# Performance work log

Hardware: AMD Instinct MI355X
Metric: run time of the kernel (lower is better)

Reference implementation:

```python
import jax, jax.numpy as jnp
import numpy as np

N_EMBD = 768
HEAD_SIZE = 72
SEQ_LEN = 512
BATCH = 64

def setup_inputs() -> dict:
    key = jax.random.key(0)
    kx, kk, kq, kv = jax.random.split(key, 4)
    # Linear weights stored as [in, out] for x @ W; torch Linear init ~ U(-1/sqrt(in), 1/sqrt(in))
    bound = 1.0 / np.sqrt(N_EMBD)
    x = jax.random.normal(kx, (BATCH, SEQ_LEN, N_EMBD), dtype=jnp.float32)
    Wk = jax.random.uniform(kk, (N_EMBD, HEAD_SIZE), minval=-bound, maxval=bound, dtype=jnp.float32)
    Wq = jax.random.uniform(kq, (N_EMBD, HEAD_SIZE), minval=-bound, maxval=bound, dtype=jnp.float32)
    Wv = jax.random.uniform(kv, (N_EMBD, HEAD_SIZE), minval=-bound, maxval=bound, dtype=jnp.float32)
    return {"x": x, "Wk": Wk, "Wq": Wq, "Wv": Wv}

def reference(x, Wk, Wq, Wv):
    # Single causal self-attention head (dropout in eval mode = identity).
    k = x @ Wk  # [B, T, H]
    q = x @ Wq  # [B, T, H]
    v = x @ Wv  # [B, T, H]
    scale = k.shape[-1] ** (-0.5)
    scores = jnp.einsum('bth,bsh->bts', q, k) * scale  # [B, T, T]
    T = scores.shape[-1]
    causal = jnp.tril(jnp.ones((T, T), dtype=bool))
    scores = jnp.where(causal, scores, -jnp.inf)
    attn = jax.nn.softmax(scores, axis=-1)
    out = jnp.einsum('bts,bsh->bth', attn, v)  # [B, T, H]
    return out
```

## Files before the change

kernel.cpp:

```cpp
#include <hip/hip_runtime.h>


typedef short bf16x8 __attribute__((ext_vector_type(8)));
typedef float f32x4 __attribute__((ext_vector_type(4)));

#define DEVI __device__ __forceinline__

DEVI unsigned f2bf(float f) {
  unsigned u = __builtin_bit_cast(unsigned, f);
  return (u + 0x7fffu + ((u >> 16) & 1u)) >> 16;
}
DEVI unsigned pk2(float a, float b) { return f2bf(a) | (f2bf(b) << 16); }

DEVI void async16(void* lds, const void* g) {
  __builtin_amdgcn_global_load_lds(
      (const __attribute__((address_space(1))) unsigned int*)g,
      (__attribute__((address_space(3))) unsigned int*)lds, 16, 0, 0);
}

__global__ __launch_bounds__(256) void cast_w_k(const float* __restrict__ Wk,
                                                const float* __restrict__ Wq,
                                                const float* __restrict__ Wv,
                                                unsigned short* __restrict__ wbt) {
  __shared__ float ldsT[72][65];
  const int mat = blockIdx.x / 12, kc = blockIdx.x % 12;
  const float* W = (mat == 0) ? Wk : (mat == 1) ? Wq : Wv;
  const float sc = (mat == 1) ? 0.11785113019775793f : 1.0f;
  const float* src = W + kc * 64 * 72;
  for (int i = threadIdx.x; i < 1152; i += 256) {
    float4 d = *(const float4*)(src + i * 4);
    int e = i * 4;
    ldsT[e % 72][e / 72] = d.x;
    ldsT[(e + 1) % 72][(e + 1) / 72] = d.y;
    ldsT[(e + 2) % 72][(e + 2) / 72] = d.z;
    ldsT[(e + 3) % 72][(e + 3) / 72] = d.w;
  }
  __syncthreads();
  for (int c = threadIdx.x; c < 640; c += 256) {
    int h = c >> 3, kb = (c & 7) * 8;
    uint4 o = {0u, 0u, 0u, 0u};
    if (h < 72) {
      const float* rowp = &ldsT[h][kb];
      o.x = pk2(rowp[0] * sc, rowp[1] * sc);
      o.y = pk2(rowp[2] * sc, rowp[3] * sc);
      o.z = pk2(rowp[4] * sc, rowp[5] * sc);
      o.w = pk2(rowp[6] * sc, rowp[7] * sc);
    }
    *(uint4*)(wbt + ((size_t)mat * 80 + h) * 768 + kc * 64 + kb) = o;
  }
}

struct ProjSmem {
  union {
    struct { short x[128 * 64]; short w[240 * 64]; } s;
    short t[80 * 136];
  };
};

__global__ __launch_bounds__(256, 2) void proj_k(
    const float* __restrict__ x, const unsigned short* __restrict__ wbt,
    unsigned short* __restrict__ Kg, unsigned short* __restrict__ Qg,
    unsigned short* __restrict__ Vt) {
  __shared__ __align__(16) ProjSmem sm;
  const int row0 = blockIdx.x * 128;
  const int tid = threadIdx.x, wave = tid >> 6, lane = tid & 63;
  const int quad = lane >> 4, l16 = lane & 15;
  const int lrow = lane >> 3, lcb = lane & 7;

  f32x4 acc[2][15] = {};

  for (int k0 = 0; k0 < 768; k0 += 64) {
#pragma unroll
    for (int i = 0; i < 8; ++i) {
      int inst = i * 4 + wave;
      if (inst < 30) {
        int r = inst * 8 + lrow;
        async16(&sm.s.w[inst * 512], wbt + (size_t)r * 768 + k0 + (lcb ^ lrow) * 8);
      }
    }
#pragma unroll
    for (int i = 0; i < 4; ++i) {
      int task = tid + 256 * i;
      int row = task >> 3, cb = task & 7;
      const float* g = x + (size_t)(row0 + row) * 768 + k0 + cb * 8;
      float4 a = *(const float4*)g;
      float4 c = *(const float4*)(g + 4);
      uint4 o = {pk2(a.x, a.y), pk2(a.z, a.w), pk2(c.x, c.y), pk2(c.z, c.w)};
      *(uint4*)&sm.s.x[row * 64 + ((cb ^ (row & 7)) * 8)] = o;
    }
    __syncthreads();
#pragma unroll
    for (int ks = 0; ks < 2; ++ks) {
      const int pblk = ((ks << 2) | quad) ^ (l16 & 7);
      bf16x8 af[2];
#pragma unroll
      for (int mt = 0; mt < 2; ++mt)
        af[mt] = *(const bf16x8*)&sm.s.x[(wave * 32 + mt * 16 + l16) * 64 + pblk * 8];
#pragma unroll
      for (int nt = 0; nt < 15; ++nt) {
        bf16x8 bf = *(const bf16x8*)&sm.s.w[(nt * 16 + l16) * 64 + pblk * 8];
        acc[0][nt] = __builtin_amdgcn_mfma_f32_16x16x32_bf16(af[0], bf, acc[0][nt], 0, 0, 0);
        acc[1][nt] = __builtin_amdgcn_mfma_f32_16x16x32_bf16(af[1], bf, acc[1][nt], 0, 0, 0);
      }
    }
    __syncthreads();
  }

#pragma unroll
  for (int gsel = 0; gsel < 2; ++gsel) {
    unsigned short* G = gsel ? Qg : Kg;
#pragma unroll
    for (int mt = 0; mt < 2; ++mt)
#pragma unroll
      for (int r = 0; r < 4; ++r) {
        size_t row = (size_t)row0 + wave * 32 + mt * 16 + quad * 4 + r;
        unsigned short* p = G + row * 104;
#pragma unroll
        for (int nt = 0; nt < 5; ++nt)
          p[nt * 16 + l16] = (unsigned short)f2bf(acc[mt][gsel * 5 + nt][r]);
        p[80 + l16] = 0;
        if (l16 < 8) p[96 + l16] = 0;
      }
  }
#pragma unroll
  for (int mt = 0; mt < 2; ++mt)
#pragma unroll
    for (int nt = 0; nt < 5; ++nt)
#pragma unroll
      for (int r = 0; r < 4; ++r)
        sm.t[(nt * 16 + l16) * 136 + wave * 32 + mt * 16 + quad * 4 + r] =
            (short)f2bf(acc[mt][10 + nt][r]);
  __syncthreads();
  int b = blockIdx.x >> 2, t0 = (blockIdx.x & 3) * 128;
  const uint4 ones = {0x3F803F80u, 0x3F803F80u, 0x3F803F80u, 0x3F803F80u};
  for (int c = tid; c < 1280; c += 256) {
    int hr = c >> 4, tc = (c & 15) * 8;
    uint4 d = *(const uint4*)&sm.t[hr * 136 + tc];
    if (hr == 72) d = ones;
    *(uint4*)(Vt + ((size_t)b * 80 + hr) * 512 + t0 + tc) = d;
  }
}

__global__ __launch_bounds__(256, 4) void attn_k(
    const unsigned short* __restrict__ Qg, const unsigned short* __restrict__ Kg,
    const unsigned short* __restrict__ Vt, float* __restrict__ out) {
  __shared__ __align__(16) short lk[64 * 104];
  __shared__ __align__(16) short lv[80 * 64];
  __shared__ __align__(16) short lp[4][16 * 72];

  int idx = (blockIdx.x < 256) ? blockIdx.x : 767 - blockIdx.x;
  const int qb = 7 - (idx >> 6), b = idx & 63;
  const int tid = threadIdx.x, wave = tid >> 6, lane = tid & 63;
  const int quad = lane >> 4, l16 = lane & 15;
  const int lrow = lane >> 3, lcb = lane & 7;
  const int trow0 = qb * 64 + wave * 16;

  bf16x8 qf[3];
#pragma unroll
  for (int kt = 0; kt < 3; ++kt)
    qf[kt] = *(const bf16x8*)(Qg + ((size_t)b * 512 + trow0 + l16) * 104 + kt * 32 + quad * 8);

  f32x4 o[5] = {};

  for (int kb = 0; kb <= qb; ++kb) {
    const int s0 = kb * 64;
    const bool diag = (kb == qb);
    const int nact = diag ? (wave + 1) : 4;

#pragma unroll
    for (int j = 0; j < 4; ++j) {
      int inst = j * 4 + wave;
      if (inst < 13)
        async16(&lk[inst * 512], Kg + ((size_t)b * 512 + s0) * 104 + inst * 512 + lane * 8);
    }
    for (int j = wave; j < 10; j += 4) {
      int r = j * 8 + lrow;
      async16(&lv[j * 512], Vt + ((size_t)b * 80 + r) * 512 + s0 + (lcb ^ lrow) * 8);
    }
    __syncthreads();

    f32x4 sacc[4] = {};
#pragma unroll
    for (int kt = 0; kt < 3; ++kt)
      for (int nt = 0; nt < nact; ++nt) {
        bf16x8 kf = *(const bf16x8*)&lk[(nt * 16 + l16) * 104 + kt * 32 + quad * 8];
        sacc[nt] = __builtin_amdgcn_mfma_f32_16x16x32_bf16(qf[kt], kf, sacc[nt], 0, 0, 0);
      }
    if (diag) {
      int nt = wave;
#pragma unroll
      for (int r = 0; r < 4; ++r) {
        int t = trow0 + quad * 4 + r;
        if (s0 + nt * 16 + l16 > t) sacc[nt][r] = -1e30f;
      }
    }
#pragma unroll
    for (int nt = 0; nt < 4; ++nt)
#pragma unroll
      for (int r = 0; r < 4; ++r) {
        float p = (nt < nact) ? __expf(sacc[nt][r]) : 0.0f;
        lp[wave][(quad * 4 + r) * 72 + nt * 16 + l16] = (short)f2bf(p);
      }
#pragma unroll
    for (int ks = 0; ks < 2; ++ks) {
      bf16x8 pf = *(const bf16x8*)&lp[wave][l16 * 72 + ks * 32 + quad * 8];
      const int pblk = ((ks << 2) | quad) ^ (l16 & 7);
#pragma unroll
      for (int nt = 0; nt < 5; ++nt) {
        bf16x8 vf = *(const bf16x8*)&lv[(nt * 16 + l16) * 64 + pblk * 8];
        o[nt] = __builtin_amdgcn_mfma_f32_16x16x32_bf16(pf, vf, o[nt], 0, 0, 0);
      }
    }
    __syncthreads();
  }

#pragma unroll
  for (int r = 0; r < 4; ++r) {
    float l = __shfl(o[4][r], (lane & 48) | 8, 64);
    float inv = 1.0f / l;
    size_t t = (size_t)b * 512 + trow0 + quad * 4 + r;
#pragma unroll
    for (int nt = 0; nt < 5; ++nt) {
      int h = nt * 16 + l16;
      if (h < 72) out[t * 72 + h] = o[nt][r] * inv;
    }
  }
}

extern "C" void kernel_launch(void* const* d_in, const int* in_sizes, int n_in,
                              void* d_out, int out_size, void* d_ws, size_t ws_size,
                              hipStream_t stream) {
  const float* x  = (const float*)d_in[0];
  const float* Wk = (const float*)d_in[1];
  const float* Wq = (const float*)d_in[2];
  const float* Wv = (const float*)d_in[3];
  float* out = (float*)d_out;

  char* ws = (char*)d_ws;
  unsigned short* Kg  = (unsigned short*)(ws);
  unsigned short* Qg  = (unsigned short*)(ws + 6815744);
  unsigned short* Vt  = (unsigned short*)(ws + 13631488);
  unsigned short* wbt = (unsigned short*)(ws + 18874368);

  cast_w_k<<<36, 256, 0, stream>>>(Wk, Wq, Wv, wbt);
  proj_k<<<256, 256, 0, stream>>>(x, wbt, Kg, Qg, Vt);
  attn_k<<<512, 256, 0, stream>>>(Qg, Kg, Vt, out);
}
```

Baseline: 193.5 us.

## Halve projection row tile and double attention key block to 128

The projection kernel now handles 64 rows per block instead of 128, launching 512 blocks so more of the GPU is busy. The attention kernel walks keys in 128-wide blocks, which halves the loop iterations and barriers, and uses a 16-way XOR swizzle for V in LDS. On the diagonal it skips MFMAs and loads past the causal limit. The cost is more LDS per attention block with occupancy lowered to 2 blocks per SM, and the projection reuses each weight tile over fewer rows.

```diff
diff --git a/kernel.cpp b/kernel.cpp
--- a/kernel.cpp
+++ b/kernel.cpp
@@ -52,8 +52,8 @@
 
 struct ProjSmem {
   union {
-    struct { short x[128 * 64]; short w[240 * 64]; } s;
-    short t[80 * 136];
+    struct { short x[64 * 64]; short w[240 * 64]; } s;
+    short t[80 * 72];
   };
 };
 
@@ -62,12 +62,12 @@
     unsigned short* __restrict__ Kg, unsigned short* __restrict__ Qg,
     unsigned short* __restrict__ Vt) {
   __shared__ __align__(16) ProjSmem sm;
-  const int row0 = blockIdx.x * 128;
+  const int row0 = blockIdx.x * 64;
   const int tid = threadIdx.x, wave = tid >> 6, lane = tid & 63;
   const int quad = lane >> 4, l16 = lane & 15;
   const int lrow = lane >> 3, lcb = lane & 7;
 
-  f32x4 acc[2][15] = {};
+  f32x4 acc[15] = {};
 
   for (int k0 = 0; k0 < 768; k0 += 64) {
 #pragma unroll
@@ -79,7 +79,7 @@
       }
     }
 #pragma unroll
-    for (int i = 0; i < 4; ++i) {
+    for (int i = 0; i < 2; ++i) {
       int task = tid + 256 * i;
       int row = task >> 3, cb = task & 7;
       const float* g = x + (size_t)(row0 + row) * 768 + k0 + cb * 8;
@@ -92,15 +92,11 @@
 #pragma unroll
     for (int ks = 0; ks < 2; ++ks) {
       const int pblk = ((ks << 2) | quad) ^ (l16 & 7);
-      bf16x8 af[2];
-#pragma unroll
-      for (int mt = 0; mt < 2; ++mt)
-        af[mt] = *(const bf16x8*)&sm.s.x[(wave * 32 + mt * 16 + l16) * 64 + pblk * 8];
+      bf16x8 af = *(const bf16x8*)&sm.s.x[(wave * 16 + l16) * 64 + pblk * 8];
 #pragma unroll
       for (int nt = 0; nt < 15; ++nt) {
         bf16x8 bf = *(const bf16x8*)&sm.s.w[(nt * 16 + l16) * 64 + pblk * 8];
-        acc[0][nt] = __builtin_amdgcn_mfma_f32_16x16x32_bf16(af[0], bf, acc[0][nt], 0, 0, 0);
-        acc[1][nt] = __builtin_amdgcn_mfma_f32_16x16x32_bf16(af[1], bf, acc[1][nt], 0, 0, 0);
+        acc[nt] = __builtin_amdgcn_mfma_f32_16x16x32_bf16(af, bf, acc[nt], 0, 0, 0);
       }
     }
     __syncthreads();
@@ -110,49 +106,44 @@
   for (int gsel = 0; gsel < 2; ++gsel) {
     unsigned short* G = gsel ? Qg : Kg;
 #pragma unroll
-    for (int mt = 0; mt < 2; ++mt)
-#pragma unroll
-      for (int r = 0; r < 4; ++r) {
-        size_t row = (size_t)row0 + wave * 32 + mt * 16 + quad * 4 + r;
-        unsigned short* p = G + row * 104;
-#pragma unroll
-        for (int nt = 0; nt < 5; ++nt)
-          p[nt * 16 + l16] = (unsigned short)f2bf(acc[mt][gsel * 5 + nt][r]);
-        p[80 + l16] = 0;
-        if (l16 < 8) p[96 + l16] = 0;
-      }
-  }
-#pragma unroll
-  for (int mt = 0; mt < 2; ++mt)
-#pragma unroll
-    for (int nt = 0; nt < 5; ++nt)
-#pragma unroll
-      for (int r = 0; r < 4; ++r)
-        sm.t[(nt * 16 + l16) * 136 + wave * 32 + mt * 16 + quad * 4 + r] =
-            (short)f2bf(acc[mt][10 + nt][r]);
+    for (int r = 0; r < 4; ++r) {
+      size_t row = (size_t)row0 + wave * 16 + quad * 4 + r;
+      unsigned short* p = G + row * 104;
+#pragma unroll
+      for (int nt = 0; nt < 5; ++nt)
+        p[nt * 16 + l16] = (unsigned short)f2bf(acc[gsel * 5 + nt][r]);
+      p[80 + l16] = 0;
+      if (l16 < 8) p[96 + l16] = 0;
+    }
+  }
+#pragma unroll
+  for (int nt = 0; nt < 5; ++nt)
+#pragma unroll
+    for (int r = 0; r < 4; ++r)
+      sm.t[(nt * 16 + l16) * 72 + wave * 16 + quad * 4 + r] =
+          (short)f2bf(acc[10 + nt][r]);
   __syncthreads();
-  int b = blockIdx.x >> 2, t0 = (blockIdx.x & 3) * 128;
+  int b = blockIdx.x >> 3, t0 = (blockIdx.x & 7) * 64;
   const uint4 ones = {0x3F803F80u, 0x3F803F80u, 0x3F803F80u, 0x3F803F80u};
-  for (int c = tid; c < 1280; c += 256) {
-    int hr = c >> 4, tc = (c & 15) * 8;
-    uint4 d = *(const uint4*)&sm.t[hr * 136 + tc];
+  for (int c = tid; c < 640; c += 256) {
+    int hr = c >> 3, tc = (c & 7) * 8;
+    uint4 d = *(const uint4*)&sm.t[hr * 72 + tc];
     if (hr == 72) d = ones;
     *(uint4*)(Vt + ((size_t)b * 80 + hr) * 512 + t0 + tc) = d;
   }
 }
 
-__global__ __launch_bounds__(256, 4) void attn_k(
+__global__ __launch_bounds__(256, 2) void attn_k(
     const unsigned short* __restrict__ Qg, const unsigned short* __restrict__ Kg,
     const unsigned short* __restrict__ Vt, float* __restrict__ out) {
-  __shared__ __align__(16) short lk[64 * 104];
-  __shared__ __align__(16) short lv[80 * 64];
-  __shared__ __align__(16) short lp[4][16 * 72];
+  __shared__ __align__(16) short lk[128 * 104];
+  __shared__ __align__(16) short lv[80 * 128];
+  __shared__ __align__(16) short lp[4][16 * 136];
 
   int idx = (blockIdx.x < 256) ? blockIdx.x : 767 - blockIdx.x;
   const int qb = 7 - (idx >> 6), b = idx & 63;
   const int tid = threadIdx.x, wave = tid >> 6, lane = tid & 63;
   const int quad = lane >> 4, l16 = lane & 15;
-  const int lrow = lane >> 3, lcb = lane & 7;
   const int trow0 = qb * 64 + wave * 16;
 
   bf16x8 qf[3];
@@ -162,55 +153,66 @@
 
   f32x4 o[5] = {};
 
-  for (int kb = 0; kb <= qb; ++kb) {
-    const int s0 = kb * 64;
-    const bool diag = (kb == qb);
-    const int nact = diag ? (wave + 1) : 4;
-
-#pragma unroll
-    for (int j = 0; j < 4; ++j) {
+  const int nkb = (qb >> 1) + 1;
+  for (int kb = 0; kb < nkb; ++kb) {
+    const int s0 = kb * 128;
+    const bool diag = (kb == (qb >> 1));
+    const int nact = diag ? ((qb & 1) * 4 + wave + 1) : 8;
+    const int kslim = diag ? ((nact + 1) >> 1) : 4;
+    const int nKinst = (diag && !(qb & 1)) ? 13 : 26;
+
+#pragma unroll
+    for (int j = 0; j < 7; ++j) {
       int inst = j * 4 + wave;
-      if (inst < 13)
+      if (inst < nKinst)
         async16(&lk[inst * 512], Kg + ((size_t)b * 512 + s0) * 104 + inst * 512 + lane * 8);
     }
-    for (int j = wave; j < 10; j += 4) {
-      int r = j * 8 + lrow;
-      async16(&lv[j * 512], Vt + ((size_t)b * 80 + r) * 512 + s0 + (lcb ^ lrow) * 8);
-    }
-    __syncthreads();
-
-    f32x4 sacc[4] = {};
+#pragma unroll
+    for (int j = 0; j < 5; ++j) {
+      int inst = j * 4 + wave;
+      int r = inst * 4 + (lane >> 4);
+      int cb = lane & 15;
+      async16(&lv[inst * 512],
+              Vt + ((size_t)b * 80 + r) * 512 + s0 + ((cb ^ (r & 15)) * 8));
+    }
+    __syncthreads();
+
+    f32x4 sacc[8] = {};
 #pragma unroll
     for (int kt = 0; kt < 3; ++kt)
-      for (int nt = 0; nt < nact; ++nt) {
-        bf16x8 kf = *(const bf16x8*)&lk[(nt * 16 + l16) * 104 + kt * 32 + quad * 8];
-        sacc[nt] = __builtin_amdgcn_mfma_f32_16x16x32_bf16(qf[kt], kf, sacc[nt], 0, 0, 0);
-      }
+#pragma unroll
+      for (int nt = 0; nt < 8; ++nt)
+        if (nt < nact) {
+          bf16x8 kf = *(const bf16x8*)&lk[(nt * 16 + l16) * 104 + kt * 32 + quad * 8];
+          sacc[nt] = __builtin_amdgcn_mfma_f32_16x16x32_bf16(qf[kt], kf, sacc[nt], 0, 0, 0);
+        }
     if (diag) {
-      int nt = wave;
-#pragma unroll
-      for (int r = 0; r < 4; ++r) {
-        int t = trow0 + quad * 4 + r;
-        if (s0 + nt * 16 + l16 > t) sacc[nt][r] = -1e30f;
-      }
-    }
-#pragma unroll
-    for (int nt = 0; nt < 4; ++nt)
+#pragma unroll
+      for (int nt = 0; nt < 8; ++nt)
+        if (nt == nact - 1)
+#pragma unroll
+          for (int r = 0; r < 4; ++r) {
+            int t = trow0 + quad * 4 + r;
+            if (s0 + nt * 16 + l16 > t) sacc[nt][r] = -1e30f;
+          }
+    }
+#pragma unroll
+    for (int nt = 0; nt < 8; ++nt)
 #pragma unroll
       for (int r = 0; r < 4; ++r) {
         float p = (nt < nact) ? __expf(sacc[nt][r]) : 0.0f;
-        lp[wave][(quad * 4 + r) * 72 + nt * 16 + l16] = (short)f2bf(p);
-      }
-#pragma unroll
-    for (int ks = 0; ks < 2; ++ks) {
-      bf16x8 pf = *(const bf16x8*)&lp[wave][l16 * 72 + ks * 32 + quad * 8];
-      const int pblk = ((ks << 2) | quad) ^ (l16 & 7);
-#pragma unroll
-      for (int nt = 0; nt < 5; ++nt) {
-        bf16x8 vf = *(const bf16x8*)&lv[(nt * 16 + l16) * 64 + pblk * 8];
-        o[nt] = __builtin_amdgcn_mfma_f32_16x16x32_bf16(pf, vf, o[nt], 0, 0, 0);
-      }
-    }
+        lp[wave][(quad * 4 + r) * 136 + nt * 16 + l16] = (short)f2bf(p);
+      }
+#pragma unroll
+    for (int ks = 0; ks < 4; ++ks)
+      if (ks < kslim) {
+        bf16x8 pf = *(const bf16x8*)&lp[wave][l16 * 136 + ks * 32 + quad * 8];
+#pragma unroll
+        for (int nt = 0; nt < 5; ++nt) {
+          bf16x8 vf = *(const bf16x8*)&lv[(nt * 16 + l16) * 128 + (((ks << 2) | quad) ^ l16) * 8];
+          o[nt] = __builtin_amdgcn_mfma_f32_16x16x32_bf16(pf, vf, o[nt], 0, 0, 0);
+        }
+      }
     __syncthreads();
   }
 
@@ -243,6 +245,6 @@
   unsigned short* wbt = (unsigned short*)(ws + 18874368);
 
   cast_w_k<<<36, 256, 0, stream>>>(Wk, Wq, Wv, wbt);
-  proj_k<<<256, 256, 0, stream>>>(x, wbt, Kg, Qg, Vt);
+  proj_k<<<512, 256, 0, stream>>>(x, wbt, Kg, Qg, Vt);
   attn_k<<<512, 256, 0, stream>>>(Qg, Kg, Vt, out);
 }
```

Measured after the change: 201.4 us. +4.1%, slower.

## Load x fragments directly from global in projection, stage weights in larger K chunks

Applied to the files above, without the earlier changes.

The projection kernel no longer stages x through LDS. Each wave now loads its x rows straight from global memory into MFMA fragments, converting them to bf16 in registers. Weights are staged in 256-wide K chunks with a 32-way XOR swizzle, so there are 3 outer iterations instead of 12 and far fewer barriers. The cost is a much larger LDS footprint (about 120KB), which drops occupancy to one block per CU. The x loads also become short, non-coalesced, latency-exposed global reads issued right before the MFMAs.

```diff
diff --git a/kernel.cpp b/kernel.cpp
--- a/kernel.cpp
+++ b/kernel.cpp
@@ -11,6 +11,11 @@
   return (u + 0x7fffu + ((u >> 16) & 1u)) >> 16;
 }
 DEVI unsigned pk2(float a, float b) { return f2bf(a) | (f2bf(b) << 16); }
+
+DEVI bf16x8 pack8(float4 a, float4 c) {
+  uint4 o = {pk2(a.x, a.y), pk2(a.z, a.w), pk2(c.x, c.y), pk2(c.z, c.w)};
+  return __builtin_bit_cast(bf16x8, o);
+}
 
 DEVI void async16(void* lds, const void* g) {
   __builtin_amdgcn_global_load_lds(
@@ -52,12 +57,12 @@
 
 struct ProjSmem {
   union {
-    struct { short x[128 * 64]; short w[240 * 64]; } s;
+    short w[240 * 256];
     short t[80 * 136];
   };
 };
 
-__global__ __launch_bounds__(256, 2) void proj_k(
+__global__ __launch_bounds__(256, 1) void proj_k(
     const float* __restrict__ x, const unsigned short* __restrict__ wbt,
     unsigned short* __restrict__ Kg, unsigned short* __restrict__ Qg,
     unsigned short* __restrict__ Vt) {
@@ -65,40 +70,35 @@
   const int row0 = blockIdx.x * 128;
   const int tid = threadIdx.x, wave = tid >> 6, lane = tid & 63;
   const int quad = lane >> 4, l16 = lane & 15;
-  const int lrow = lane >> 3, lcb = lane & 7;
+  const int wr = wave * 32;
 
   f32x4 acc[2][15] = {};
 
-  for (int k0 = 0; k0 < 768; k0 += 64) {
-#pragma unroll
-    for (int i = 0; i < 8; ++i) {
-      int inst = i * 4 + wave;
-      if (inst < 30) {
-        int r = inst * 8 + lrow;
-        async16(&sm.s.w[inst * 512], wbt + (size_t)r * 768 + k0 + (lcb ^ lrow) * 8);
-      }
-    }
-#pragma unroll
-    for (int i = 0; i < 4; ++i) {
-      int task = tid + 256 * i;
-      int row = task >> 3, cb = task & 7;
-      const float* g = x + (size_t)(row0 + row) * 768 + k0 + cb * 8;
-      float4 a = *(const float4*)g;
-      float4 c = *(const float4*)(g + 4);
-      uint4 o = {pk2(a.x, a.y), pk2(a.z, a.w), pk2(c.x, c.y), pk2(c.z, c.w)};
-      *(uint4*)&sm.s.x[row * 64 + ((cb ^ (row & 7)) * 8)] = o;
-    }
-    __syncthreads();
-#pragma unroll
-    for (int ks = 0; ks < 2; ++ks) {
-      const int pblk = ((ks << 2) | quad) ^ (l16 & 7);
+  for (int kc = 0; kc < 3; ++kc) {
+    const int kbase = kc * 256;
+#pragma unroll
+    for (int j = 0; j < 30; ++j) {
+      int inst = j * 4 + wave;
+      int r = 2 * inst + (lane >> 5);
+      int cb = lane & 31;
+      async16(&sm.w[inst * 512],
+              wbt + (size_t)r * 768 + kbase + ((cb ^ (r & 31)) * 8));
+    }
+    __syncthreads();
+#pragma unroll
+    for (int ks = 0; ks < 8; ++ks) {
       bf16x8 af[2];
 #pragma unroll
-      for (int mt = 0; mt < 2; ++mt)
-        af[mt] = *(const bf16x8*)&sm.s.x[(wave * 32 + mt * 16 + l16) * 64 + pblk * 8];
+      for (int mt = 0; mt < 2; ++mt) {
+        const float* g = x + (size_t)(row0 + wr + mt * 16 + l16) * 768 +
+                         kbase + ks * 32 + quad * 8;
+        af[mt] = pack8(*(const float4*)g, *(const float4*)(g + 4));
+      }
 #pragma unroll
       for (int nt = 0; nt < 15; ++nt) {
-        bf16x8 bf = *(const bf16x8*)&sm.s.w[(nt * 16 + l16) * 64 + pblk * 8];
+        int row = nt * 16 + l16;
+        bf16x8 bf = *(const bf16x8*)&sm.w[row * 256 +
+                                          (((ks * 4 + quad) ^ (row & 31)) * 8)];
         acc[0][nt] = __builtin_amdgcn_mfma_f32_16x16x32_bf16(af[0], bf, acc[0][nt], 0, 0, 0);
         acc[1][nt] = __builtin_amdgcn_mfma_f32_16x16x32_bf16(af[1], bf, acc[1][nt], 0, 0, 0);
       }
@@ -113,7 +113,7 @@
     for (int mt = 0; mt < 2; ++mt)
 #pragma unroll
       for (int r = 0; r < 4; ++r) {
-        size_t row = (size_t)row0 + wave * 32 + mt * 16 + quad * 4 + r;
+        size_t row = (size_t)row0 + wr + mt * 16 + quad * 4 + r;
         unsigned short* p = G + row * 104;
 #pragma unroll
         for (int nt = 0; nt < 5; ++nt)
@@ -128,7 +128,7 @@
     for (int nt = 0; nt < 5; ++nt)
 #pragma unroll
       for (int r = 0; r < 4; ++r)
-        sm.t[(nt * 16 + l16) * 136 + wave * 32 + mt * 16 + quad * 4 + r] =
+        sm.t[(nt * 16 + l16) * 136 + wr + mt * 16 + quad * 4 + r] =
             (short)f2bf(acc[mt][10 + nt][r]);
   __syncthreads();
   int b = blockIdx.x >> 2, t0 = (blockIdx.x & 3) * 128;
```

After: 205.8 us. 6.4% more time.

## Halve projection row tile and split waves across M and N

Applied to the files above, without the earlier changes.

The projection kernel now processes 64 rows per block instead of 128 and splits the four waves into two row groups and two column groups of output tiles. The grid doubles to 512 blocks, giving more parallelism and lower per-wave register use on a GPU with many CUs. In exchange, the weight tile is loaded into LDS by twice as many blocks, adding global and L2 traffic. The epilogue is reworked so each wave writes its own K, Q or V columns, with V transposed through a smaller LDS buffer.

```diff
diff --git a/kernel.cpp b/kernel.cpp
--- a/kernel.cpp
+++ b/kernel.cpp
@@ -52,8 +52,8 @@
 
 struct ProjSmem {
   union {
-    struct { short x[128 * 64]; short w[240 * 64]; } s;
-    short t[80 * 136];
+    struct { short x[64 * 64]; short w[240 * 64]; } s;
+    short t[80 * 72];
   };
 };
 
@@ -62,12 +62,14 @@
     unsigned short* __restrict__ Kg, unsigned short* __restrict__ Qg,
     unsigned short* __restrict__ Vt) {
   __shared__ __align__(16) ProjSmem sm;
-  const int row0 = blockIdx.x * 128;
+  const int row0 = blockIdx.x * 64;
   const int tid = threadIdx.x, wave = tid >> 6, lane = tid & 63;
   const int quad = lane >> 4, l16 = lane & 15;
   const int lrow = lane >> 3, lcb = lane & 7;
-
-  f32x4 acc[2][15] = {};
+  const int mg = wave >> 1, ng = wave & 1;
+  const int ntile0 = ng * 8, ntn = ng ? 7 : 8;
+
+  f32x4 acc[2][8] = {};
 
   for (int k0 = 0; k0 < 768; k0 += 64) {
 #pragma unroll
@@ -79,7 +81,7 @@
       }
     }
 #pragma unroll
-    for (int i = 0; i < 4; ++i) {
+    for (int i = 0; i < 2; ++i) {
       int task = tid + 256 * i;
       int row = task >> 3, cb = task & 7;
       const float* g = x + (size_t)(row0 + row) * 768 + k0 + cb * 8;
@@ -95,47 +97,48 @@
       bf16x8 af[2];
 #pragma unroll
       for (int mt = 0; mt < 2; ++mt)
-        af[mt] = *(const bf16x8*)&sm.s.x[(wave * 32 + mt * 16 + l16) * 64 + pblk * 8];
-#pragma unroll
-      for (int nt = 0; nt < 15; ++nt) {
-        bf16x8 bf = *(const bf16x8*)&sm.s.w[(nt * 16 + l16) * 64 + pblk * 8];
-        acc[0][nt] = __builtin_amdgcn_mfma_f32_16x16x32_bf16(af[0], bf, acc[0][nt], 0, 0, 0);
-        acc[1][nt] = __builtin_amdgcn_mfma_f32_16x16x32_bf16(af[1], bf, acc[1][nt], 0, 0, 0);
-      }
-    }
-    __syncthreads();
-  }
-
-#pragma unroll
-  for (int gsel = 0; gsel < 2; ++gsel) {
-    unsigned short* G = gsel ? Qg : Kg;
-#pragma unroll
-    for (int mt = 0; mt < 2; ++mt)
-#pragma unroll
-      for (int r = 0; r < 4; ++r) {
-        size_t row = (size_t)row0 + wave * 32 + mt * 16 + quad * 4 + r;
-        unsigned short* p = G + row * 104;
-#pragma unroll
-        for (int nt = 0; nt < 5; ++nt)
-          p[nt * 16 + l16] = (unsigned short)f2bf(acc[mt][gsel * 5 + nt][r]);
-        p[80 + l16] = 0;
-        if (l16 < 8) p[96 + l16] = 0;
-      }
-  }
+        af[mt] = *(const bf16x8*)&sm.s.x[(mg * 32 + mt * 16 + l16) * 64 + pblk * 8];
+#pragma unroll
+      for (int j = 0; j < 8; ++j)
+        if (j < ntn) {
+          int nt = ntile0 + j;
+          bf16x8 bf = *(const bf16x8*)&sm.s.w[(nt * 16 + l16) * 64 + pblk * 8];
+          acc[0][j] = __builtin_amdgcn_mfma_f32_16x16x32_bf16(af[0], bf, acc[0][j], 0, 0, 0);
+          acc[1][j] = __builtin_amdgcn_mfma_f32_16x16x32_bf16(af[1], bf, acc[1][j], 0, 0, 0);
+        }
+    }
+    __syncthreads();
+  }
+
 #pragma unroll
   for (int mt = 0; mt < 2; ++mt)
 #pragma unroll
-    for (int nt = 0; nt < 5; ++nt)
-#pragma unroll
-      for (int r = 0; r < 4; ++r)
-        sm.t[(nt * 16 + l16) * 136 + wave * 32 + mt * 16 + quad * 4 + r] =
-            (short)f2bf(acc[mt][10 + nt][r]);
+    for (int r = 0; r < 4; ++r) {
+      int lrow64 = mg * 32 + mt * 16 + quad * 4 + r;
+      size_t grow = (size_t)row0 + lrow64;
+#pragma unroll
+      for (int j = 0; j < 8; ++j)
+        if (j < ntn) {
+          int nt = ntile0 + j;
+          float v = acc[mt][j][r];
+          if (nt < 5) {
+            Kg[grow * 104 + nt * 16 + l16] = (unsigned short)f2bf(v);
+          } else if (nt < 10) {
+            Qg[grow * 104 + (nt - 5) * 16 + l16] = (unsigned short)f2bf(v);
+          } else {
+            sm.t[((nt - 10) * 16 + l16) * 72 + lrow64] = (short)f2bf(v);
+          }
+        }
+      unsigned short* p = (ng ? Qg : Kg) + grow * 104;
+      p[80 + l16] = 0;
+      if (l16 < 8) p[96 + l16] = 0;
+    }
   __syncthreads();
-  int b = blockIdx.x >> 2, t0 = (blockIdx.x & 3) * 128;
+  int b = blockIdx.x >> 3, t0 = (blockIdx.x & 7) * 64;
   const uint4 ones = {0x3F803F80u, 0x3F803F80u, 0x3F803F80u, 0x3F803F80u};
-  for (int c = tid; c < 1280; c += 256) {
-    int hr = c >> 4, tc = (c & 15) * 8;
-    uint4 d = *(const uint4*)&sm.t[hr * 136 + tc];
+  for (int c = tid; c < 640; c += 256) {
+    int hr = c >> 3, tc = (c & 7) * 8;
+    uint4 d = *(const uint4*)&sm.t[hr * 72 + tc];
     if (hr == 72) d = ones;
     *(uint4*)(Vt + ((size_t)b * 80 + hr) * 512 + t0 + tc) = d;
   }
@@ -243,6 +246,6 @@
   unsigned short* wbt = (unsigned short*)(ws + 18874368);
 
   cast_w_k<<<36, 256, 0, stream>>>(Wk, Wq, Wv, wbt);
-  proj_k<<<256, 256, 0, stream>>>(x, wbt, Kg, Qg, Vt);
+  proj_k<<<512, 256, 0, stream>>>(x, wbt, Kg, Qg, Vt);
   attn_k<<<512, 256, 0, stream>>>(Qg, Kg, Vt, out);
 }
```

Measured after the change: 193.0 us. About the same (-0.3%).
